# Kernel optimization log

Measured on AMD Instinct MI355X. Metric: run time of the kernel, lower is better.

The kernel has to match this reference:

```python
import jax, jax.numpy as jnp
import numpy as np

T, B, C, H, W = 128, 16, 4, 84, 84
NUM_ACTIONS, FEAT, HID = 18, 512, 256


def _conv(x, w, b, stride):
    # x: (N,C,H,W), w: (O,I,kh,kw)
    y = jax.lax.conv_general_dilated(
        x, w, window_strides=(stride, stride), padding='VALID',
        dimension_numbers=('NCHW', 'OIHW', 'NCHW'))
    return y + b[None, :, None, None]


def setup_inputs() -> dict:
    key = jax.random.key(0)
    ks = jax.random.split(key, 24)
    s = 0.05
    inp = {
        'obs_seq': jax.random.uniform(ks[0], (T, B, C, H, W), jnp.float32) * 255.0,
        'actions_seq': jax.random.randint(ks[1], (T, B), 0, NUM_ACTIONS),
        'episode_starts_seq': jax.random.randint(ks[2], (T, B), 0, 2).astype(jnp.float32),
        'h0': jnp.zeros((1, B, HID), jnp.float32),
        'c0': jnp.zeros((1, B, HID), jnp.float32),
        # NatureCNN params
        'conv1_w': jax.random.normal(ks[3], (32, C, 8, 8)) * s,
        'conv1_b': jnp.zeros((32,)),
        'conv2_w': jax.random.normal(ks[4], (64, 32, 4, 4)) * s,
        'conv2_b': jnp.zeros((64,)),
        'conv3_w': jax.random.normal(ks[5], (64, 64, 3, 3)) * s,
        'conv3_b': jnp.zeros((64,)),
        'fc_w': jax.random.normal(ks[6], (FEAT, 64 * 7 * 7)) * s,
        'fc_b': jnp.zeros((FEAT,)),
        # LSTM params (torch gate order i,f,g,o)
        'w_ih': jax.random.normal(ks[7], (4 * HID, FEAT)) * s,
        'w_hh': jax.random.normal(ks[8], (4 * HID, HID)) * s,
        'b_ih': jnp.zeros((4 * HID,)),
        'b_hh': jnp.zeros((4 * HID,)),
        # heads
        'actor_w': jax.random.normal(ks[9], (NUM_ACTIONS, HID)) * 0.01,
        'actor_b': jnp.zeros((NUM_ACTIONS,)),
        'critic_w': jax.random.normal(ks[10], (1, HID)) * s,
        'critic_b': jnp.zeros((1,)),
        'aux_w': jax.random.normal(ks[11], (1, FEAT)) * s,
        'aux_b': jnp.zeros((1,)),
    }
    return inp


def reference(obs_seq, actions_seq, episode_starts_seq, h0, c0,
              conv1_w, conv1_b, conv2_w, conv2_b, conv3_w, conv3_b,
              fc_w, fc_b, w_ih, w_hh, b_ih, b_hh,
              actor_w, actor_b, critic_w, critic_b, aux_w, aux_b):
    t, b = actions_seq.shape
    x = obs_seq.reshape(t * b, *obs_seq.shape[2:]) / 255.0
    x = jax.nn.relu(_conv(x, conv1_w, conv1_b, 4))   # (TB,32,20,20)
    x = jax.nn.relu(_conv(x, conv2_w, conv2_b, 2))   # (TB,64,9,9)
    x = jax.nn.relu(_conv(x, conv3_w, conv3_b, 1))   # (TB,64,7,7)
    feat = jax.nn.relu(x.reshape(t * b, -1) @ fc_w.T + fc_b)  # (TB,FEAT)

    aux_logits = (feat @ aux_w.T + aux_b).squeeze(-1).reshape(t, b)
    feat_seq = feat.reshape(t, b, -1)

    def step(carry, inp):
        h, c = carry
        x_t, s_t = inp
        keep = (1.0 - s_t)[:, None]
        h = h * keep
        c = c * keep
        gates = x_t @ w_ih.T + b_ih + h @ w_hh.T + b_hh  # (B,4H)
        i, f, g, o = jnp.split(gates, 4, axis=-1)
        c = jax.nn.sigmoid(f) * c + jax.nn.sigmoid(i) * jnp.tanh(g)
        h = jax.nn.sigmoid(o) * jnp.tanh(c)
        return (h, c), h

    _, out = jax.lax.scan(step, (h0[0], c0[0]), (feat_seq, episode_starts_seq))  # (T,B,HID)

    logits = out @ actor_w.T + actor_b
    logp = jax.nn.log_softmax(logits, axis=-1)
    log_probs = jnp.take_along_axis(logp, actions_seq[..., None], axis=-1).squeeze(-1)
    entropy = -jnp.sum(jnp.exp(logp) * logp, axis=-1)
    values = (out @ critic_w.T + critic_b).squeeze(-1)
    return log_probs, entropy, values, aux_logits
```

## Files before the change

kernel.cpp:

```cpp
#include <hip/hip_runtime.h>
#include <hip/hip_bf16.h>
#include <cstddef>

typedef __attribute__((ext_vector_type(8))) short bf16x8;
typedef __attribute__((ext_vector_type(8))) unsigned short u16x8;
typedef __attribute__((ext_vector_type(4))) float f32x4;

static constexpr size_t OFF_X1B   = 0;
static constexpr size_t OFF_X2B   = 52428800;
static constexpr size_t OFF_X3B   = 73662464;
static constexpr size_t OFF_FEATB = 86507520;
static constexpr size_t OFF_W2B   = 88604672;
static constexpr size_t OFF_W3B   = 88670208;
static constexpr size_t OFF_FCWB  = 88743936;
static constexpr size_t OFF_WIHB  = 91955200;
static constexpr size_t OFF_GX    = 97198080;
static constexpr size_t OFF_HSEQ  = 105586688;
static constexpr size_t OFF_W1B   = 108732416;
static constexpr size_t OFF_WHHB  = 108748800;
static constexpr size_t OFF_ORDB  = 109273088;
static constexpr size_t OFF_ORDT0 = 109281280;
static constexpr size_t OFF_ORDLEN= 109289472;
static constexpr size_t OFF_NSEG  = 109297664;
static constexpr size_t OFF_FCPART= 109305856;

__device__ __forceinline__ float sigmoidf_(float x) {
  return 1.0f / (1.0f + __expf(-x));
}
__device__ __forceinline__ float tanhf_(float x) {
  return 1.0f - 2.0f / (__expf(2.0f * x) + 1.0f);
}
__device__ __forceinline__ unsigned short f2bfu(float x) {
  union { __hip_bfloat16 b; unsigned short u; } cv;
  cv.b = __float2bfloat16(x);
  return cv.u;
}

__global__ __launch_bounds__(256) void prep_kernel(
    const float* __restrict__ c1w, const float* __restrict__ c2w,
    const float* __restrict__ c3w, const float* __restrict__ fcw,
    const float* __restrict__ wih, const float* __restrict__ whh,
    __hip_bfloat16* __restrict__ w1b,
    __hip_bfloat16* __restrict__ w2b, __hip_bfloat16* __restrict__ w3b,
    __hip_bfloat16* __restrict__ fcwb, __hip_bfloat16* __restrict__ wihb,
    __hip_bfloat16* __restrict__ whhb) {
  int i = blockIdx.x * 256 + threadIdx.x;
  if (i < 32768) {
    int o = i >> 9, k = i & 511;
    int pos = k >> 5, ci = k & 31;
    int ky = pos >> 2, kx = pos & 3;
    w2b[i] = __float2bfloat16(c2w[o * 512 + ci * 16 + ky * 4 + kx]);
  } else if (i < 69632) {
    int j = i - 32768;
    int o = j / 576, k = j - o * 576;
    int pos = k >> 6, ci = k & 63;
    int ky = pos / 3, kx = pos - ky * 3;
    w3b[j] = __float2bfloat16(c3w[o * 576 + ci * 9 + ky * 3 + kx]);
  } else if (i < 1675264) {
    int j = i - 69632;
    int o = j / 3136, k = j - o * 3136;
    int sp = k >> 6, ci = k & 63;
    fcwb[j] = __float2bfloat16(fcw[o * 3136 + ci * 49 + sp]);
  } else if (i < 2199552) {
    int j = i - 1675264;
    wihb[j] = __float2bfloat16(wih[j]);
  } else if (i < 2461696) {
    int j = i - 2199552;
    whhb[j] = __float2bfloat16(whh[j]);
  } else if (i < 2469888) {
    int j = i - 2461696;
    int oc = j >> 8, k = j & 255;
    int ky = k >> 5, rem = k & 31;
    int ci = rem >> 3, kx = rem & 7;
    w1b[j] = __float2bfloat16(c1w[oc * 256 + ci * 64 + ky * 8 + kx] * (1.0f / 255.0f));
  }
}

__global__ __launch_bounds__(256) void plan_kernel(
    const float* __restrict__ starts, int* __restrict__ ord_b,
    int* __restrict__ ord_t0, int* __restrict__ ord_len,
    int* __restrict__ nseg_out) {
  __shared__ float s_starts[2048];
  __shared__ int s_t0[2048];
  __shared__ int s_len[2048];
  __shared__ int cnt[16];
  __shared__ int hist[132];
  __shared__ int off[132];
  const int tid = threadIdx.x;
  {
    float4* d = (float4*)s_starts;
    const float4* s = (const float4*)starts;
#pragma unroll
    for (int i = 0; i < 2; ++i) d[tid + i * 256] = s[tid + i * 256];
  }
  if (tid < 132) hist[tid] = 0;
  __syncthreads();
  if (tid < 16) {
    int b = tid, c = 0;
    for (int t = 0; t < 128; ++t) {
      float s = s_starts[t * 16 + b];
      if (t == 0 || s != 0.0f) {
        if (c > 0) s_len[b * 128 + c - 1] = t - s_t0[b * 128 + c - 1];
        s_t0[b * 128 + c] = t;
        ++c;
      }
    }
    s_len[b * 128 + c - 1] = 128 - s_t0[b * 128 + c - 1];
    cnt[b] = c;
  }
  __syncthreads();
  for (int idx = tid; idx < 2048; idx += 256) {
    int b = idx >> 7, i = idx & 127;
    if (i < cnt[b]) atomicAdd(&hist[s_len[idx]], 1);
  }
  __syncthreads();
  if (tid == 0) {
    int running = 0;
    for (int L = 128; L >= 1; --L) { off[L] = running; running += hist[L]; }
    *nseg_out = running;
  }
  __syncthreads();
  for (int idx = tid; idx < 2048; idx += 256) {
    int b = idx >> 7, i = idx & 127;
    if (i < cnt[b]) {
      int len = s_len[idx];
      int pos = atomicAdd(&off[len], 1);
      ord_b[pos] = b;
      ord_t0[pos] = s_t0[idx];
      ord_len[pos] = len;
    }
  }
}

__global__ __launch_bounds__(256) void conv1_mfma(
    const float* __restrict__ obs, const __hip_bfloat16* __restrict__ w1b,
    const float* __restrict__ b1, __hip_bfloat16* __restrict__ x1b) {
  constexpr int LDK = 40;
  __shared__ __align__(16) __hip_bfloat16 As[128 * LDK];
  __shared__ __align__(16) __hip_bfloat16 Ws[32 * LDK];
  const int tid = threadIdx.x;
  const int m0 = blockIdx.x * 128;
  const int l = tid & 63;
  const int wv = tid >> 6;
  const int lane16 = l & 15;
  const int quad = l >> 4;
  const int m_base = wv * 32;

  f32x4 acc[2][2] = {};

  const float* arow[2];
  int arw[2], acp[2];
#pragma unroll
  for (int c = 0; c < 2; ++c) {
    const int id = tid + c * 256;
    const int row = id >> 2, cpos = id & 3;
    arw[c] = row; acp[c] = cpos;
    const int m = m0 + row;
    const int n = m / 400, sp = m - n * 400;
    const int oy = sp / 20, ox = sp - oy * 20;
    arow[c] = obs + (size_t)n * 28224 + cpos * 7056 + (oy * 4) * 84 + ox * 4;
  }
  const int wrow = tid >> 2, wcp = tid & 3;
  const __hip_bfloat16* wsrc = w1b + wrow * 256 + wcp * 8;

  for (int s = 0; s < 8; ++s) {
    float4 p[2], q[2];
#pragma unroll
    for (int c = 0; c < 2; ++c) {
      const float* r = arow[c] + s * 84;
      p[c] = *(const float4*)r;
      q[c] = *(const float4*)(r + 4);
    }
    uint4 wval;
    if (tid < 128) wval = *(const uint4*)(wsrc + s * 32);
    __syncthreads();
#pragma unroll
    for (int c = 0; c < 2; ++c) {
      u16x8 v;
      v[0] = f2bfu(p[c].x); v[1] = f2bfu(p[c].y);
      v[2] = f2bfu(p[c].z); v[3] = f2bfu(p[c].w);
      v[4] = f2bfu(q[c].x); v[5] = f2bfu(q[c].y);
      v[6] = f2bfu(q[c].z); v[7] = f2bfu(q[c].w);
      *(u16x8*)&As[arw[c] * LDK + acp[c] * 8] = v;
    }
    if (tid < 128) *(uint4*)&Ws[wrow * LDK + wcp * 8] = wval;
    __syncthreads();
    const bf16x8 a0 = *(const bf16x8*)&As[(m_base + lane16) * LDK + quad * 8];
    const bf16x8 a1 = *(const bf16x8*)&As[(m_base + 16 + lane16) * LDK + quad * 8];
#pragma unroll
    for (int nf = 0; nf < 2; ++nf) {
      const bf16x8 b = *(const bf16x8*)&Ws[(nf * 16 + lane16) * LDK + quad * 8];
      acc[0][nf] = __builtin_amdgcn_mfma_f32_16x16x32_bf16(a0, b, acc[0][nf], 0, 0, 0);
      acc[1][nf] = __builtin_amdgcn_mfma_f32_16x16x32_bf16(a1, b, acc[1][nf], 0, 0, 0);
    }
  }
#pragma unroll
  for (int nf = 0; nf < 2; ++nf) {
    const int col = nf * 16 + lane16;
    const float bb = b1[col];
#pragma unroll
    for (int mf = 0; mf < 2; ++mf) {
#pragma unroll
      for (int r = 0; r < 4; ++r) {
        const int row = m0 + m_base + mf * 16 + quad * 4 + r;
        const float v = fmaxf(acc[mf][nf][r] + bb, 0.f);
        x1b[(size_t)row * 32 + col] = __float2bfloat16(v);
      }
    }
  }
}

template<int BM, int MODE>
__global__ __launch_bounds__(256) void gemm_mfma(
    const __hip_bfloat16* __restrict__ Abase,
    const __hip_bfloat16* __restrict__ Wb,
    const float* __restrict__ bias1, const float* __restrict__ bias2,
    float* __restrict__ Cf, __hip_bfloat16* __restrict__ Cb,
    const int M, const int N, const int K, const int relu,
    float* __restrict__ Cpart) {
  constexpr int LDK = 40;
  __shared__ __align__(16) __hip_bfloat16 As[BM * LDK];
  __shared__ __align__(16) __hip_bfloat16 Ws[64 * LDK];
  const int tid = threadIdx.x;
  const int m0 = blockIdx.y * BM;
  const int n0 = blockIdx.x * 64;
  const int l = tid & 63;
  const int wv = tid >> 6;
  const int lane16 = l & 15;
  const int quad = l >> 4;
  constexpr int NF = (BM == 128) ? 4 : 2;
  const int m_base = (BM == 128) ? wv * 32 : (wv & 1) * 32;
  const int n_base = (BM == 128) ? 0 : (wv >> 1) * 32;
  constexpr int NCA = (BM == 128) ? 2 : 1;

  f32x4 acc[2][NF] = {};

  const __hip_bfloat16* arow[NCA];
  int acp[NCA];
#pragma unroll
  for (int c = 0; c < NCA; ++c) {
    const int id = tid + c * 256;
    const int row = id >> 2, cpos = id & 3;
    const int m = m0 + row;
    acp[c] = cpos;
    if (MODE == 0) {
      arow[c] = Abase + (size_t)m * K + cpos * 8;
    } else if (MODE == 1) {
      const int n = m / 81, sp = m - n * 81;
      const int oy = sp / 9, ox = sp - oy * 9;
      arow[c] = Abase + ((n * 20 + oy * 2) * 20 + ox * 2) * 32 + cpos * 8;
    } else {
      const int n = m / 49, sp = m - n * 49;
      const int oy = sp / 7, ox = sp - oy * 7;
      arow[c] = Abase + ((n * 9 + oy) * 9 + ox) * 64 + cpos * 8;
    }
  }
  const int wrow = tid >> 2, wcp = tid & 3;
  const __hip_bfloat16* wsrc = Wb + (size_t)(n0 + wrow) * K + wcp * 8;

  int s0 = 0, s1 = K >> 5;
  if (Cpart) {
    const int total = K >> 5;
    const int zz = blockIdx.z;
    const int q = total >> 2, rr = total & 3;
    s0 = zz * q + (zz < rr ? zz : rr);
    s1 = s0 + q + (zz < rr ? 1 : 0);
  }
  for (int s = s0; s < s1; ++s) {
    uint4 av[NCA];
#pragma unroll
    for (int c = 0; c < NCA; ++c) {
      const __hip_bfloat16* p;
      if (MODE == 0) {
        p = arow[c] + s * 32;
      } else if (MODE == 1) {
        p = arow[c] + ((s >> 2) * 20 + (s & 3)) * 32;
      } else {
        const int pos = s >> 1;
        const int ky = pos / 3, kx = pos - ky * 3;
        p = arow[c] + (ky * 9 + kx) * 64 + (s & 1) * 32;
      }
      av[c] = *(const uint4*)p;
    }
    const uint4 wval = *(const uint4*)(wsrc + s * 32);
    __syncthreads();
#pragma unroll
    for (int c = 0; c < NCA; ++c) {
      const int row = (tid + c * 256) >> 2;
      *(uint4*)&As[row * LDK + acp[c] * 8] = av[c];
    }
    *(uint4*)&Ws[wrow * LDK + wcp * 8] = wval;
    __syncthreads();
    const bf16x8 a0 = *(const bf16x8*)&As[(m_base + lane16) * LDK + quad * 8];
    const bf16x8 a1 = *(const bf16x8*)&As[(m_base + 16 + lane16) * LDK + quad * 8];
#pragma unroll
    for (int nf = 0; nf < NF; ++nf) {
      const bf16x8 b = *(const bf16x8*)&Ws[(n_base + nf * 16 + lane16) * LDK + quad * 8];
      acc[0][nf] = __builtin_amdgcn_mfma_f32_16x16x32_bf16(a0, b, acc[0][nf], 0, 0, 0);
      acc[1][nf] = __builtin_amdgcn_mfma_f32_16x16x32_bf16(a1, b, acc[1][nf], 0, 0, 0);
    }
  }
  if (Cpart) {
    float* dst = Cpart + (size_t)blockIdx.z * M * N;
#pragma unroll
    for (int nf = 0; nf < NF; ++nf) {
      const int col = n0 + n_base + nf * 16 + lane16;
#pragma unroll
      for (int mf = 0; mf < 2; ++mf) {
#pragma unroll
        for (int r = 0; r < 4; ++r) {
          const int row = m0 + m_base + mf * 16 + quad * 4 + r;
          dst[(size_t)row * N + col] = acc[mf][nf][r];
        }
      }
    }
    return;
  }
#pragma unroll
  for (int nf = 0; nf < NF; ++nf) {
    const int col = n0 + n_base + nf * 16 + lane16;
    float bb = bias1[col];
    if (bias2) bb += bias2[col];
#pragma unroll
    for (int mf = 0; mf < 2; ++mf) {
#pragma unroll
      for (int r = 0; r < 4; ++r) {
        const int row = m0 + m_base + mf * 16 + quad * 4 + r;
        float v = acc[mf][nf][r] + bb;
        if (relu) v = fmaxf(v, 0.f);
        if (Cf) Cf[(size_t)row * N + col] = v;
        if (Cb) Cb[(size_t)row * N + col] = __float2bfloat16(v);
      }
    }
  }
}

__global__ __launch_bounds__(256) void fc_reduce(
    const float* __restrict__ part, const float* __restrict__ fcb,
    const float* __restrict__ aux_w, const float* __restrict__ aux_b,
    __hip_bfloat16* __restrict__ featb, float* __restrict__ outp) {
  const int row = blockIdx.x;
  const int tid = threadIdx.x;
  __shared__ float red[256];
  float auxacc = 0.f;
#pragma unroll
  for (int h = 0; h < 2; ++h) {
    const int c = tid + h * 256;
    const size_t base = (size_t)row * 512 + c;
    float v = part[base] + part[1048576 + base] + part[2097152 + base] +
              part[3145728 + base];
    v += fcb[c];
    v = fmaxf(v, 0.f);
    featb[base] = __float2bfloat16(v);
    auxacc += v * aux_w[c];
  }
  red[tid] = auxacc;
  __syncthreads();
  for (int s = 128; s > 0; s >>= 1) {
    if (tid < s) red[tid] += red[tid + s];
    __syncthreads();
  }
  if (tid == 0) outp[6144 + row] = red[0] + aux_b[0];
}

__global__ __launch_bounds__(1024, 4) void lstm_mfma(
    const float* __restrict__ gx, const __hip_bfloat16* __restrict__ whhb,
    const float* __restrict__ starts, const float* __restrict__ h0,
    const float* __restrict__ c0, const int* __restrict__ ord_b,
    const int* __restrict__ ord_t0, const int* __restrict__ ord_len,
    const int* __restrict__ nseg_p, float* __restrict__ hseq) {
  constexpr int LDH = 264;
  constexpr int PS  = 1028;
  __shared__ __align__(16) __hip_bfloat16 h_lds[16 * LDH];
  __shared__ __align__(16) float pre[16 * PS];
  __shared__ int sg_b[16], sg_t0[16], sg_len[16];
  const int g = blockIdx.x;
  const int nseg = *nseg_p;
  if (g * 16 >= nseg) return;
  const int tid = threadIdx.x;
  const int wv = tid >> 6;
  const int l = tid & 63;
  const int lane16 = l & 15, quad = l >> 4;
  if (tid < 16) {
    const int s = g * 16 + tid;
    sg_b[tid] = (s < nseg) ? ord_b[s] : 0;
    sg_t0[tid] = (s < nseg) ? ord_t0[s] : 0;
    sg_len[tid] = (s < nseg) ? ord_len[s] : 0;
  }
  __syncthreads();
  bf16x8 bfrag[2][8];
#pragma unroll
  for (int nt = 0; nt < 2; ++nt)
#pragma unroll
    for (int ks = 0; ks < 8; ++ks)
      bfrag[nt][ks] = *(const bf16x8*)&whhb[
          (size_t)(wv * 64 + nt * 16 + lane16) * 256 + ks * 32 + quad * 8];
  const __hip_bfloat16* bs2 = &whhb[(size_t)(wv * 64 + 32 + lane16) * 256 + quad * 8];
  const __hip_bfloat16* bs3 = &whhb[(size_t)(wv * 64 + 48 + lane16) * 256 + quad * 8];

  const int m_own = wv;
  const int u = l * 4;
  const int b_own = sg_b[m_own];
  const int t0_own = sg_t0[m_own];
  const int len_own = sg_len[m_own];
  float4 c_reg = make_float4(0.f, 0.f, 0.f, 0.f);
  {
    float4 hv = make_float4(0.f, 0.f, 0.f, 0.f);
    if (len_own > 0 && t0_own == 0) {
      const float keep = 1.0f - starts[b_own];
      const float4 h4 = *(const float4*)&h0[b_own * 256 + u];
      const float4 c4 = *(const float4*)&c0[b_own * 256 + u];
      hv = make_float4(h4.x * keep, h4.y * keep, h4.z * keep, h4.w * keep);
      c_reg = make_float4(c4.x * keep, c4.y * keep, c4.z * keep, c4.w * keep);
    }
    __hip_bfloat16* hd = &h_lds[m_own * LDH + u];
    hd[0] = __float2bfloat16(hv.x); hd[1] = __float2bfloat16(hv.y);
    hd[2] = __float2bfloat16(hv.z); hd[3] = __float2bfloat16(hv.w);
  }
  const int maxlen = sg_len[0];
  for (int tt = 0; tt < maxlen; ++tt) {
    __syncthreads();
    f32x4 acc[4] = {};
#pragma unroll
    for (int ks = 0; ks < 8; ++ks) {
      const bf16x8 b2 = *(const bf16x8*)(bs2 + ks * 32);
      const bf16x8 b3 = *(const bf16x8*)(bs3 + ks * 32);
      const bf16x8 a = *(const bf16x8*)&h_lds[lane16 * LDH + ks * 32 + quad * 8];
      acc[0] = __builtin_amdgcn_mfma_f32_16x16x32_bf16(a, bfrag[0][ks], acc[0], 0, 0, 0);
      acc[1] = __builtin_amdgcn_mfma_f32_16x16x32_bf16(a, bfrag[1][ks], acc[1], 0, 0, 0);
      acc[2] = __builtin_amdgcn_mfma_f32_16x16x32_bf16(a, b2, acc[2], 0, 0, 0);
      acc[3] = __builtin_amdgcn_mfma_f32_16x16x32_bf16(a, b3, acc[3], 0, 0, 0);
    }
#pragma unroll
    for (int nt = 0; nt < 4; ++nt)
#pragma unroll
      for (int r = 0; r < 4; ++r)
        pre[(quad * 4 + r) * PS + wv * 64 + nt * 16 + lane16] = acc[nt][r];
    __syncthreads();
    if (tt < len_own) {
      const int t = t0_own + tt;
      const size_t gbase = (size_t)(t * 16 + b_own) * 1024 + u;
      const float4 g0 = *(const float4*)&gx[gbase];
      const float4 g1 = *(const float4*)&gx[gbase + 256];
      const float4 g2 = *(const float4*)&gx[gbase + 512];
      const float4 g3 = *(const float4*)&gx[gbase + 768];
      const float4 p0 = *(const float4*)&pre[m_own * PS + u];
      const float4 p1 = *(const float4*)&pre[m_own * PS + u + 256];
      const float4 p2 = *(const float4*)&pre[m_own * PS + u + 512];
      const float4 p3 = *(const float4*)&pre[m_own * PS + u + 768];
      const float i0 = sigmoidf_(p0.x + g0.x), i1 = sigmoidf_(p0.y + g0.y),
                  i2 = sigmoidf_(p0.z + g0.z), i3 = sigmoidf_(p0.w + g0.w);
      const float f0 = sigmoidf_(p1.x + g1.x), f1 = sigmoidf_(p1.y + g1.y),
                  f2 = sigmoidf_(p1.z + g1.z), f3 = sigmoidf_(p1.w + g1.w);
      const float q0 = tanhf_(p2.x + g2.x), q1 = tanhf_(p2.y + g2.y),
                  q2 = tanhf_(p2.z + g2.z), q3 = tanhf_(p2.w + g2.w);
      const float o0 = sigmoidf_(p3.x + g3.x), o1 = sigmoidf_(p3.y + g3.y),
                  o2 = sigmoidf_(p3.z + g3.z), o3 = sigmoidf_(p3.w + g3.w);
      c_reg.x = fmaf(f0, c_reg.x, i0 * q0);
      c_reg.y = fmaf(f1, c_reg.y, i1 * q1);
      c_reg.z = fmaf(f2, c_reg.z, i2 * q2);
      c_reg.w = fmaf(f3, c_reg.w, i3 * q3);
      const float4 h4 = make_float4(o0 * tanhf_(c_reg.x), o1 * tanhf_(c_reg.y),
                                    o2 * tanhf_(c_reg.z), o3 * tanhf_(c_reg.w));
      __hip_bfloat16* hd = &h_lds[m_own * LDH + u];
      hd[0] = __float2bfloat16(h4.x); hd[1] = __float2bfloat16(h4.y);
      hd[2] = __float2bfloat16(h4.z); hd[3] = __float2bfloat16(h4.w);
      *(float4*)&hseq[(size_t)(t * 16 + b_own) * 256 + u] = h4;
    }
  }
}

__global__ __launch_bounds__(256) void heads_kernel(
    const float* __restrict__ hseq, const int* __restrict__ actions,
    const float* __restrict__ actor_w, const float* __restrict__ actor_b,
    const float* __restrict__ critic_w, const float* __restrict__ critic_b,
    float* __restrict__ outp) {
  const int tid = threadIdx.x;
  const int wv = tid >> 6, l = tid & 63;
  const int tb = blockIdx.x * 4 + wv;
  const float4 h4 = *(const float4*)&hseq[(size_t)tb * 256 + l * 4];
  float part[19];
#pragma unroll
  for (int o = 0; o < 18; ++o) {
    const float4 w = *(const float4*)&actor_w[o * 256 + l * 4];
    part[o] = h4.x * w.x + h4.y * w.y + h4.z * w.z + h4.w * w.w;
  }
  {
    const float4 w = *(const float4*)&critic_w[l * 4];
    part[18] = h4.x * w.x + h4.y * w.y + h4.z * w.z + h4.w * w.w;
  }
#pragma unroll
  for (int off = 32; off > 0; off >>= 1) {
#pragma unroll
    for (int o = 0; o < 19; ++o) part[o] += __shfl_xor(part[o], off);
  }
  float lg[18];
  float m = -1e30f;
#pragma unroll
  for (int o = 0; o < 18; ++o) {
    lg[o] = part[o] + actor_b[o];
    m = fmaxf(m, lg[o]);
  }
  float se = 0.f;
#pragma unroll
  for (int o = 0; o < 18; ++o) se += __expf(lg[o] - m);
  const float lse = __logf(se);
  float ent = 0.f;
#pragma unroll
  for (int o = 0; o < 18; ++o) {
    const float lp = lg[o] - m - lse;
    ent -= __expf(lp) * lp;
  }
  if (l == 0) {
    const int a = actions[tb];
    outp[tb] = lg[a] - m - lse;
    outp[2048 + tb] = ent;
    outp[4096 + tb] = part[18] + critic_b[0];
  }
}

extern "C" void kernel_launch(void* const* d_in, const int* in_sizes, int n_in,
                              void* d_out, int out_size, void* d_ws, size_t ws_size,
                              hipStream_t stream) {
  const float* obs     = (const float*)d_in[0];
  const int*   actions = (const int*)d_in[1];
  const float* starts  = (const float*)d_in[2];
  const float* h0      = (const float*)d_in[3];
  const float* c0      = (const float*)d_in[4];
  const float* c1w     = (const float*)d_in[5];
  const float* c1b     = (const float*)d_in[6];
  const float* c2w     = (const float*)d_in[7];
  const float* c2b     = (const float*)d_in[8];
  const float* c3w     = (const float*)d_in[9];
  const float* c3b     = (const float*)d_in[10];
  const float* fcw     = (const float*)d_in[11];
  const float* fcb     = (const float*)d_in[12];
  const float* wih     = (const float*)d_in[13];
  const float* whh     = (const float*)d_in[14];
  const float* bih     = (const float*)d_in[15];
  const float* bhh     = (const float*)d_in[16];
  const float* aw      = (const float*)d_in[17];
  const float* ab      = (const float*)d_in[18];
  const float* cw      = (const float*)d_in[19];
  const float* cb      = (const float*)d_in[20];
  const float* auxw    = (const float*)d_in[21];
  const float* auxb    = (const float*)d_in[22];

  char* ws = (char*)d_ws;
  __hip_bfloat16* x1b   = (__hip_bfloat16*)(ws + OFF_X1B);
  __hip_bfloat16* x2b   = (__hip_bfloat16*)(ws + OFF_X2B);
  __hip_bfloat16* x3b   = (__hip_bfloat16*)(ws + OFF_X3B);
  __hip_bfloat16* featb = (__hip_bfloat16*)(ws + OFF_FEATB);
  __hip_bfloat16* w2b   = (__hip_bfloat16*)(ws + OFF_W2B);
  __hip_bfloat16* w3b   = (__hip_bfloat16*)(ws + OFF_W3B);
  __hip_bfloat16* fcwb  = (__hip_bfloat16*)(ws + OFF_FCWB);
  __hip_bfloat16* wihb  = (__hip_bfloat16*)(ws + OFF_WIHB);
  __hip_bfloat16* w1b   = (__hip_bfloat16*)(ws + OFF_W1B);
  __hip_bfloat16* whhb  = (__hip_bfloat16*)(ws + OFF_WHHB);
  float* gx   = (float*)(ws + OFF_GX);
  float* hseq = (float*)(ws + OFF_HSEQ);
  int* ord_b   = (int*)(ws + OFF_ORDB);
  int* ord_t0  = (int*)(ws + OFF_ORDT0);
  int* ord_len = (int*)(ws + OFF_ORDLEN);
  int* nseg    = (int*)(ws + OFF_NSEG);
  float* fcpart= (float*)(ws + OFF_FCPART);
  float* outp = (float*)d_out;

  prep_kernel<<<9648, 256, 0, stream>>>(c1w, c2w, c3w, fcw, wih, whh,
                                        w1b, w2b, w3b, fcwb, wihb, whhb);
  plan_kernel<<<1, 256, 0, stream>>>(starts, ord_b, ord_t0, ord_len, nseg);
  conv1_mfma<<<6400, 256, 0, stream>>>(obs, w1b, c1b, x1b);
  gemm_mfma<128, 1><<<dim3(1, 1296), 256, 0, stream>>>(
      x1b, w2b, c2b, nullptr, nullptr, x2b, 165888, 64, 512, 1, nullptr);
  gemm_mfma<128, 2><<<dim3(1, 784), 256, 0, stream>>>(
      x2b, w3b, c3b, nullptr, nullptr, x3b, 100352, 64, 576, 1, nullptr);
  gemm_mfma<64, 0><<<dim3(8, 32, 4), 256, 0, stream>>>(
      x3b, fcwb, fcb, nullptr, nullptr, nullptr, 2048, 512, 3136, 0, fcpart);
  fc_reduce<<<2048, 256, 0, stream>>>(fcpart, fcb, auxw, auxb, featb, outp);
  gemm_mfma<64, 0><<<dim3(16, 32), 256, 0, stream>>>(
      featb, wihb, bih, bhh, gx, nullptr, 2048, 1024, 512, 0, nullptr);
  lstm_mfma<<<128, 1024, 0, stream>>>(gx, whhb, starts, h0, c0,
                                      ord_b, ord_t0, ord_len, nseg, hseq);
  heads_kernel<<<512, 256, 0, stream>>>(hseq, actions, aw, ab, cw, cb, outp);
}
```

Measured before the change: 722.5 us.

## Load conv A-operands directly into registers, keep whole weights in LDS

```diff
diff --git a/kernel.cpp b/kernel.cpp
--- a/kernel.cpp
+++ b/kernel.cpp
@@ -30,10 +30,10 @@
 __device__ __forceinline__ float tanhf_(float x) {
   return 1.0f - 2.0f / (__expf(2.0f * x) + 1.0f);
 }
-__device__ __forceinline__ unsigned short f2bfu(float x) {
-  union { __hip_bfloat16 b; unsigned short u; } cv;
+__device__ __forceinline__ short f2bfs(float x) {
+  union { __hip_bfloat16 b; short s; } cv;
   cv.b = __float2bfloat16(x);
-  return cv.u;
+  return cv.s;
 }
 
 __global__ __launch_bounds__(256) void prep_kernel(
@@ -132,66 +132,44 @@
   }
 }
 
-__global__ __launch_bounds__(256) void conv1_mfma(
+__global__ __launch_bounds__(256, 2) void conv1_rs(
     const float* __restrict__ obs, const __hip_bfloat16* __restrict__ w1b,
     const float* __restrict__ b1, __hip_bfloat16* __restrict__ x1b) {
-  constexpr int LDK = 40;
-  __shared__ __align__(16) __hip_bfloat16 As[128 * LDK];
-  __shared__ __align__(16) __hip_bfloat16 Ws[32 * LDK];
+  constexpr int LDW = 264;
+  __shared__ __align__(16) __hip_bfloat16 Ws[32 * LDW];
   const int tid = threadIdx.x;
-  const int m0 = blockIdx.x * 128;
-  const int l = tid & 63;
-  const int wv = tid >> 6;
-  const int lane16 = l & 15;
-  const int quad = l >> 4;
-  const int m_base = wv * 32;
-
-  f32x4 acc[2][2] = {};
-
-  const float* arow[2];
-  int arw[2], acp[2];
-#pragma unroll
-  for (int c = 0; c < 2; ++c) {
-    const int id = tid + c * 256;
-    const int row = id >> 2, cpos = id & 3;
-    arw[c] = row; acp[c] = cpos;
-    const int m = m0 + row;
+  const int wv = tid >> 6, l = tid & 63;
+  const int lane16 = l & 15, quad = l >> 4;
+  for (int i = tid; i < 1024; i += 256) {
+    const int r = i >> 5, c = (i & 31) * 8;
+    *(uint4*)&Ws[r * LDW + c] = *(const uint4*)&w1b[r * 256 + c];
+  }
+  const int m0 = blockIdx.x * 256 + wv * 64;
+  const float* abase[4];
+#pragma unroll
+  for (int mf = 0; mf < 4; ++mf) {
+    const int m = m0 + mf * 16 + lane16;
     const int n = m / 400, sp = m - n * 400;
     const int oy = sp / 20, ox = sp - oy * 20;
-    arow[c] = obs + (size_t)n * 28224 + cpos * 7056 + (oy * 4) * 84 + ox * 4;
-  }
-  const int wrow = tid >> 2, wcp = tid & 3;
-  const __hip_bfloat16* wsrc = w1b + wrow * 256 + wcp * 8;
-
+    abase[mf] = obs + (size_t)n * 28224 + quad * 7056 + (oy * 4) * 84 + ox * 4;
+  }
+  f32x4 acc[4][2] = {};
+  __syncthreads();
+#pragma unroll 2
   for (int s = 0; s < 8; ++s) {
-    float4 p[2], q[2];
-#pragma unroll
-    for (int c = 0; c < 2; ++c) {
-      const float* r = arow[c] + s * 84;
-      p[c] = *(const float4*)r;
-      q[c] = *(const float4*)(r + 4);
-    }
-    uint4 wval;
-    if (tid < 128) wval = *(const uint4*)(wsrc + s * 32);
-    __syncthreads();
-#pragma unroll
-    for (int c = 0; c < 2; ++c) {
-      u16x8 v;
-      v[0] = f2bfu(p[c].x); v[1] = f2bfu(p[c].y);
-      v[2] = f2bfu(p[c].z); v[3] = f2bfu(p[c].w);
-      v[4] = f2bfu(q[c].x); v[5] = f2bfu(q[c].y);
-      v[6] = f2bfu(q[c].z); v[7] = f2bfu(q[c].w);
-      *(u16x8*)&As[arw[c] * LDK + acp[c] * 8] = v;
-    }
-    if (tid < 128) *(uint4*)&Ws[wrow * LDK + wcp * 8] = wval;
-    __syncthreads();
-    const bf16x8 a0 = *(const bf16x8*)&As[(m_base + lane16) * LDK + quad * 8];
-    const bf16x8 a1 = *(const bf16x8*)&As[(m_base + 16 + lane16) * LDK + quad * 8];
-#pragma unroll
-    for (int nf = 0; nf < 2; ++nf) {
-      const bf16x8 b = *(const bf16x8*)&Ws[(nf * 16 + lane16) * LDK + quad * 8];
-      acc[0][nf] = __builtin_amdgcn_mfma_f32_16x16x32_bf16(a0, b, acc[0][nf], 0, 0, 0);
-      acc[1][nf] = __builtin_amdgcn_mfma_f32_16x16x32_bf16(a1, b, acc[1][nf], 0, 0, 0);
+    bf16x8 bfr[2];
+#pragma unroll
+    for (int nf = 0; nf < 2; ++nf)
+      bfr[nf] = *(const bf16x8*)&Ws[(nf * 16 + lane16) * LDW + s * 32 + quad * 8];
+#pragma unroll
+    for (int mf = 0; mf < 4; ++mf) {
+      const float4 p = *(const float4*)(abase[mf] + s * 84);
+      const float4 q = *(const float4*)(abase[mf] + s * 84 + 4);
+      bf16x8 a;
+      a[0] = f2bfs(p.x); a[1] = f2bfs(p.y); a[2] = f2bfs(p.z); a[3] = f2bfs(p.w);
+      a[4] = f2bfs(q.x); a[5] = f2bfs(q.y); a[6] = f2bfs(q.z); a[7] = f2bfs(q.w);
+      acc[mf][0] = __builtin_amdgcn_mfma_f32_16x16x32_bf16(a, bfr[0], acc[mf][0], 0, 0, 0);
+      acc[mf][1] = __builtin_amdgcn_mfma_f32_16x16x32_bf16(a, bfr[1], acc[mf][1], 0, 0, 0);
     }
   }
 #pragma unroll
@@ -199,14 +177,82 @@
     const int col = nf * 16 + lane16;
     const float bb = b1[col];
 #pragma unroll
-    for (int mf = 0; mf < 2; ++mf) {
+    for (int mf = 0; mf < 4; ++mf)
 #pragma unroll
       for (int r = 0; r < 4; ++r) {
-        const int row = m0 + m_base + mf * 16 + quad * 4 + r;
-        const float v = fmaxf(acc[mf][nf][r] + bb, 0.f);
-        x1b[(size_t)row * 32 + col] = __float2bfloat16(v);
+        const int row = m0 + mf * 16 + quad * 4 + r;
+        x1b[(size_t)row * 32 + col] =
+            __float2bfloat16(fmaxf(acc[mf][nf][r] + bb, 0.f));
       }
-    }
+  }
+}
+
+template<int KK, int LDW, int MODE>
+__global__ __launch_bounds__(256, 2) void conv_rs(
+    const __hip_bfloat16* __restrict__ A, const __hip_bfloat16* __restrict__ Wb,
+    const float* __restrict__ bias, __hip_bfloat16* __restrict__ Cb) {
+  __shared__ __align__(16) __hip_bfloat16 Ws[64 * LDW];
+  const int tid = threadIdx.x;
+  const int wv = tid >> 6, l = tid & 63;
+  const int lane16 = l & 15, quad = l >> 4;
+  constexpr int CPR = KK / 8;
+  constexpr int CH = 64 * CPR;
+  for (int i = tid; i < CH; i += 256) {
+    const int r = i / CPR;
+    const int c = (i - r * CPR) * 8;
+    *(uint4*)&Ws[r * LDW + c] = *(const uint4*)&Wb[r * KK + c];
+  }
+  const int m0 = blockIdx.x * 256 + wv * 64;
+  const __hip_bfloat16* abase[4];
+#pragma unroll
+  for (int mf = 0; mf < 4; ++mf) {
+    const int m = m0 + mf * 16 + lane16;
+    if (MODE == 1) {
+      const int n = m / 81, sp = m - n * 81;
+      const int oy = sp / 9, ox = sp - oy * 9;
+      abase[mf] = A + ((n * 20 + oy * 2) * 20 + ox * 2) * 32 + quad * 8;
+    } else {
+      const int n = m / 49, sp = m - n * 49;
+      const int oy = sp / 7, ox = sp - oy * 7;
+      abase[mf] = A + ((n * 9 + oy) * 9 + ox) * 64 + quad * 8;
+    }
+  }
+  f32x4 acc[4][4] = {};
+  __syncthreads();
+  constexpr int KS = KK / 32;
+#pragma unroll
+  for (int s = 0; s < KS; ++s) {
+    int koff;
+    if (MODE == 1) {
+      koff = ((s >> 2) * 20 + (s & 3)) * 32;
+    } else {
+      const int pos = s >> 1;
+      koff = ((pos / 3) * 9 + (pos % 3)) * 64 + (s & 1) * 32;
+    }
+    bf16x8 bfr[4];
+#pragma unroll
+    for (int nf = 0; nf < 4; ++nf)
+      bfr[nf] = *(const bf16x8*)&Ws[(nf * 16 + lane16) * LDW + s * 32 + quad * 8];
+#pragma unroll
+    for (int mf = 0; mf < 4; ++mf) {
+      const bf16x8 a = *(const bf16x8*)(abase[mf] + koff);
+#pragma unroll
+      for (int nf = 0; nf < 4; ++nf)
+        acc[mf][nf] = __builtin_amdgcn_mfma_f32_16x16x32_bf16(a, bfr[nf], acc[mf][nf], 0, 0, 0);
+    }
+  }
+#pragma unroll
+  for (int nf = 0; nf < 4; ++nf) {
+    const int col = nf * 16 + lane16;
+    const float bb = bias[col];
+#pragma unroll
+    for (int mf = 0; mf < 4; ++mf)
+#pragma unroll
+      for (int r = 0; r < 4; ++r) {
+        const int row = m0 + mf * 16 + quad * 4 + r;
+        Cb[(size_t)row * 64 + col] =
+            __float2bfloat16(fmaxf(acc[mf][nf][r] + bb, 0.f));
+      }
   }
 }
 
@@ -243,17 +289,7 @@
     const int row = id >> 2, cpos = id & 3;
     const int m = m0 + row;
     acp[c] = cpos;
-    if (MODE == 0) {
-      arow[c] = Abase + (size_t)m * K + cpos * 8;
-    } else if (MODE == 1) {
-      const int n = m / 81, sp = m - n * 81;
-      const int oy = sp / 9, ox = sp - oy * 9;
-      arow[c] = Abase + ((n * 20 + oy * 2) * 20 + ox * 2) * 32 + cpos * 8;
-    } else {
-      const int n = m / 49, sp = m - n * 49;
-      const int oy = sp / 7, ox = sp - oy * 7;
-      arow[c] = Abase + ((n * 9 + oy) * 9 + ox) * 64 + cpos * 8;
-    }
+    arow[c] = Abase + (size_t)m * K + cpos * 8;
   }
   const int wrow = tid >> 2, wcp = tid & 3;
   const __hip_bfloat16* wsrc = Wb + (size_t)(n0 + wrow) * K + wcp * 8;
@@ -270,17 +306,7 @@
     uint4 av[NCA];
 #pragma unroll
     for (int c = 0; c < NCA; ++c) {
-      const __hip_bfloat16* p;
-      if (MODE == 0) {
-        p = arow[c] + s * 32;
-      } else if (MODE == 1) {
-        p = arow[c] + ((s >> 2) * 20 + (s & 3)) * 32;
-      } else {
-        const int pos = s >> 1;
-        const int ky = pos / 3, kx = pos - ky * 3;
-        p = arow[c] + (ky * 9 + kx) * 64 + (s & 1) * 32;
-      }
-      av[c] = *(const uint4*)p;
+      av[c] = *(const uint4*)(arow[c] + s * 32);
     }
     const uint4 wval = *(const uint4*)(wsrc + s * 32);
     __syncthreads();
@@ -569,11 +595,9 @@
   prep_kernel<<<9648, 256, 0, stream>>>(c1w, c2w, c3w, fcw, wih, whh,
                                         w1b, w2b, w3b, fcwb, wihb, whhb);
   plan_kernel<<<1, 256, 0, stream>>>(starts, ord_b, ord_t0, ord_len, nseg);
-  conv1_mfma<<<6400, 256, 0, stream>>>(obs, w1b, c1b, x1b);
-  gemm_mfma<128, 1><<<dim3(1, 1296), 256, 0, stream>>>(
-      x1b, w2b, c2b, nullptr, nullptr, x2b, 165888, 64, 512, 1, nullptr);
-  gemm_mfma<128, 2><<<dim3(1, 784), 256, 0, stream>>>(
-      x2b, w3b, c3b, nullptr, nullptr, x3b, 100352, 64, 576, 1, nullptr);
+  conv1_rs<<<3200, 256, 0, stream>>>(obs, w1b, c1b, x1b);
+  conv_rs<512, 520, 1><<<648, 256, 0, stream>>>(x1b, w2b, c2b, x2b);
+  conv_rs<576, 584, 2><<<392, 256, 0, stream>>>(x2b, w3b, c3b, x3b);
   gemm_mfma<64, 0><<<dim3(8, 32, 4), 256, 0, stream>>>(
       x3b, fcwb, fcb, nullptr, nullptr, nullptr, 2048, 512, 3136, 0, fcpart);
   fc_reduce<<<2048, 256, 0, stream>>>(fcpart, fcb, auxw, auxb, featb, outp);
```

Result: faster. 688.9 us (-4.6%).
